# Kernel tuning notes

Measured on AMD Instinct MI355X. Metric: run time of the kernel, lower is better.

## Reference

```python
import jax, jax.numpy as jnp
import numpy as np

EPS = 1e-8  # F.cosine_similarity default eps
THRESHOLD = 0.5
NUM_PROTOTYPES = 64
W_DIV_ZP = 1.0
W_DIV_PZ = 1.0
W_DIV_PP = 1.0
W_NUM = 1.0
W_CLUSTER = 1.0
W_SEP = 1.0  # NOTE: original forward applies this weight to cluster_loss (upstream bug), replicated here


def setup_inputs() -> dict:
    key = jax.random.key(0)
    k1, k2, k3, k4, k5 = jax.random.split(key, 5)
    N, IN_DIM, P, D = 4096, 768, NUM_PROTOTYPES, 256
    x = jax.random.normal(k1, (N, IN_DIM), dtype=jnp.float32)
    labels = jax.random.randint(k2, (N,), 0, 2, dtype=jnp.int64)
    # nn.Linear(input_dim, prototype_dim): W stored as [D, IN] in torch; use [IN, D] for x @ W
    bound = 1.0 / np.sqrt(IN_DIM)
    W = jax.random.uniform(k3, (IN_DIM, D), minval=-bound, maxval=bound, dtype=jnp.float32)
    b = jax.random.uniform(k4, (D,), minval=-bound, maxval=bound, dtype=jnp.float32)
    prototypes = jax.random.normal(k5, (P, D), dtype=jnp.float32)
    return {"x": x, "labels": labels, "W": W, "b": b, "prototypes": prototypes}


def _cdist(a, b):
    # Euclidean pairwise distances [Na, Nb]
    d2 = (jnp.sum(a * a, -1)[:, None] + jnp.sum(b * b, -1)[None, :]
          - 2.0 * (a @ b.T))
    return jnp.sqrt(jnp.maximum(d2, 0.0))


def _forward(x, labels, W, b, prototypes):
    P = prototypes.shape[0]
    P_pos = P // 2
    z = x @ W + b  # [N, D]

    zn = z / jnp.maximum(jnp.linalg.norm(z, axis=-1, keepdims=True), EPS)
    pn = prototypes / jnp.maximum(jnp.linalg.norm(prototypes, axis=-1, keepdims=True), EPS)
    cos = zn @ pn.T  # [N, P] cosine similarities

    token_sequences = cos[:, :, None] * prototypes[None, :, :]  # [N, P, D]

    dist = _cdist(z, prototypes)  # [N, P]

    # diversity_loss_z_p: nearest sample per prototype
    ni = jnp.argmin(dist, axis=0)  # [P]
    l_zp = jnp.mean(jnp.linalg.norm(z[ni] - prototypes, axis=-1))

    # diversity_loss_p_z: nearest prototype per sample (intended semantics)
    nj = jnp.argmin(dist, axis=1)  # [N]
    l_pz = jnp.mean(jnp.linalg.norm(z - prototypes[nj], axis=-1))

    # diversity_loss_p_p: mean pairwise prototype distance excluding diagonal
    pp = _cdist(prototypes, prototypes)
    off = 1.0 - jnp.eye(P, dtype=pp.dtype)
    l_pp = jnp.sum(pp * off) / (P * (P - 1))

    # loss_num_prototypes: penalize samples similar to > P/4 prototypes
    num_sim = jnp.sum((cos > THRESHOLD).astype(jnp.float32), axis=1)
    l_num = jnp.sum((num_sim > P / 4).astype(jnp.float32))

    # cluster_loss: 1 - max similarity to own-class prototypes, mean over all samples
    max_pos = jnp.max(cos[:, :P_pos], axis=1)
    max_neg = jnp.max(cos[:, P_pos:], axis=1)
    d_cl = jnp.where(labels == 1, 1.0 - max_pos, 1.0 - max_neg)
    l_cluster = jnp.mean(d_cl)

    loss = (W_DIV_ZP * l_zp + W_DIV_PZ * l_pz + W_DIV_PP * l_pp
            + W_NUM * l_num + W_CLUSTER * l_cluster + W_SEP * l_cluster)
    return token_sequences, loss


def reference(x, labels, W, b, prototypes):
    return _forward(x, labels, W, b, prototypes)
```

## Files before the change

kernel.cpp:

```cpp
#include <hip/hip_runtime.h>

#define NS 4096
#define IND 768
#define PP 64
#define DD 256
#define EPSF 1e-8f
#define KHALF 384

typedef float f32x4 __attribute__((ext_vector_type(4)));

__global__ __launch_bounds__(256) void k_pre(const float* __restrict__ x,
                                             const float* __restrict__ W,
                                             const float* __restrict__ protos,
                                             float* __restrict__ z0,
                                             float* __restrict__ z1,
                                             float* __restrict__ pnorm,
                                             float* __restrict__ ppsum,
                                             unsigned int* __restrict__ minu,
                                             float* __restrict__ accum) {
    __shared__ float As[16][68];
    __shared__ float Bs[16][68];
    int tid = threadIdx.x;
    int bid = blockIdx.x;

    if (bid >= 512) {
        int p = bid - 512;
        int lane = tid & 63, w = tid >> 6;
        if (w == 0) {
            float s = 0.f;
            for (int d = lane; d < DD; d += 64) { float v = protos[p * DD + d]; s += v * v; }
#pragma unroll
            for (int o = 1; o < 64; o <<= 1) s += __shfl_xor(s, o);
            if (lane == 0) pnorm[p] = sqrtf(s);
        }
        int q = tid >> 2, quarter = tid & 3;
        const float* pr = protos + p * DD + quarter * 64;
        const float* qr = protos + q * DD + quarter * 64;
        float s2 = 0.f;
        for (int d = 0; d < 64; ++d) { float diff = pr[d] - qr[d]; s2 += diff * diff; }
        s2 += __shfl_xor(s2, 1);
        s2 += __shfl_xor(s2, 2);
        float contrib = (quarter == 0 && q != p) ? sqrtf(s2) : 0.f;
#pragma unroll
        for (int o = 1; o < 64; o <<= 1) contrib += __shfl_xor(contrib, o);
        float* red = &As[0][0];
        if (lane == 0) red[w] = contrib;
        __syncthreads();
        if (tid == 0) {
            ppsum[p] = red[0] + red[1] + red[2] + red[3];
            minu[p] = 0xFFFFFFFFu;
            if (p == 0) {
                accum[0] = 0.f; accum[1] = 0.f; accum[2] = 0.f;
                ((unsigned int*)accum)[3] = 0u;
            }
        }
        return;
    }

    int bx = bid & 63, by = (bid >> 6) & 3, bz = bid >> 8;
    int m0 = bx * 64, n0 = by * 64, kbase = bz * KHALF;
    float* __restrict__ zout = bz ? z1 : z0;
    float c[4][4] = {};
    int tx = tid & 15, ty = tid >> 4;
    int am = tid >> 2, ak = (tid & 3) * 4;
    int bk = tid >> 4, bn = (tid & 15) * 4;
    const float* xp = x + (size_t)(m0 + am) * IND + kbase + ak;
    const float* wp = W + (size_t)(kbase + bk) * DD + n0 + bn;

    f32x4 ra = *(const f32x4*)xp;
    f32x4 rb = *(const f32x4*)wp;

    for (int k0 = 0; k0 < KHALF; k0 += 16) {
        As[ak + 0][am] = ra.x;
        As[ak + 1][am] = ra.y;
        As[ak + 2][am] = ra.z;
        As[ak + 3][am] = ra.w;
        *(f32x4*)&Bs[bk][bn] = rb;
        __syncthreads();
        if (k0 + 16 < KHALF) {
            ra = *(const f32x4*)(xp + k0 + 16);
            rb = *(const f32x4*)(wp + (size_t)(k0 + 16) * DD);
        }
#pragma unroll
        for (int k = 0; k < 16; ++k) {
            float a[4], bb[4];
#pragma unroll
            for (int i = 0; i < 4; ++i) a[i] = As[k][ty * 4 + i];
#pragma unroll
            for (int j = 0; j < 4; ++j) bb[j] = Bs[k][tx * 4 + j];
#pragma unroll
            for (int i = 0; i < 4; ++i)
#pragma unroll
                for (int j = 0; j < 4; ++j) c[i][j] += a[i] * bb[j];
        }
        __syncthreads();
    }
#pragma unroll
    for (int i = 0; i < 4; ++i) {
        int m = m0 + ty * 4 + i;
        f32x4 rv = {c[i][0], c[i][1], c[i][2], c[i][3]};
        *(f32x4*)&zout[(size_t)m * DD + n0 + tx * 4] = rv;
    }
}

__global__ __launch_bounds__(256) void k_cosw(const float* __restrict__ z0,
                                              const float* __restrict__ z1,
                                              const float* __restrict__ bias,
                                              const float* __restrict__ protos,
                                              const float* __restrict__ pnorm,
                                              const int* __restrict__ labels,
                                              float* __restrict__ out,
                                              unsigned int* __restrict__ minu,
                                              float* __restrict__ accum,
                                              const float* __restrict__ ppsum,
                                              int out_last) {
    __shared__ f32x4 protoT4[PP * 64];
    __shared__ __align__(16) float rowbuf[4][2][DD];
    __shared__ float wmin[4][64];
    __shared__ float wacc[4][3];
    int tid = threadIdx.x;
    const f32x4* pr4g = (const f32x4*)protos;
    for (int idx = tid; idx < PP * 64; idx += 256) {
        int pp = idx >> 6, db = idx & 63;
        protoT4[pp * 64 + (db ^ (pp & 7))] = pr4g[idx];
    }

    int w = tid >> 6, lane = tid & 63;
    int p = lane;
    float pn = pnorm[p];
    float pn2 = pn * pn;
    float4 b4 = ((const float4*)bias)[lane];
    int nbase = blockIdx.x * 8 + w * 2;

    float zn[2];
#pragma unroll
    for (int s = 0; s < 2; ++s) {
        int n = nbase + s;
        float4 a = ((const float4*)z0)[n * 64 + lane];
        float4 cc = ((const float4*)z1)[n * 64 + lane];
        float4 r;
        r.x = a.x + cc.x + b4.x; r.y = a.y + cc.y + b4.y;
        r.z = a.z + cc.z + b4.z; r.w = a.w + cc.w + b4.w;
        float ss = r.x * r.x + r.y * r.y + r.z * r.z + r.w * r.w;
#pragma unroll
        for (int o = 1; o < 64; o <<= 1) ss += __shfl_xor(ss, o);
        zn[s] = sqrtf(ss);
        ((float4*)rowbuf[w][s])[lane] = r;
    }
    __syncthreads();

    float dot0 = 0.f, dot1 = 0.f;
#pragma unroll 8
    for (int d4 = 0; d4 < 64; ++d4) {
        f32x4 r0 = ((const f32x4*)rowbuf[w][0])[d4];
        f32x4 r1 = ((const f32x4*)rowbuf[w][1])[d4];
        f32x4 pv = protoT4[p * 64 + (d4 ^ (p & 7))];
        dot0 += r0.x * pv.x + r0.y * pv.y + r0.z * pv.z + r0.w * pv.w;
        dot1 += r1.x * pv.x + r1.y * pv.y + r1.z * pv.z + r1.w * pv.w;
    }
    float dots[2] = {dot0, dot1};

    float cosv[2];
    float regmin = 3.4e38f;
    float s_pz = 0.f, s_cl = 0.f, s_num = 0.f;
#pragma unroll
    for (int s = 0; s < 2; ++s) {
        int n = nbase + s;
        float dot = dots[s];
        float c = dot / (fmaxf(zn[s], EPSF) * fmaxf(pn, EPSF));
        cosv[s] = c;
        float d2 = zn[s] * zn[s] + pn2 - 2.f * dot;
        float dist = sqrtf(fmaxf(d2, 0.f));
        regmin = fminf(regmin, dist);

        unsigned long long bal = __ballot(c > 0.5f);
        int cnt = __popcll(bal);

        float mind = dist;
#pragma unroll
        for (int o = 1; o < 64; o <<= 1) mind = fminf(mind, __shfl_xor(mind, o));
        float mx = c;
#pragma unroll
        for (int o = 1; o < 32; o <<= 1) mx = fmaxf(mx, __shfl_xor(mx, o));
        float max_pos = __shfl(mx, 0);
        float max_neg = __shfl(mx, 32);
        if (lane == 0) {
            float dcl = (labels[n] == 1) ? (1.f - max_pos) : (1.f - max_neg);
            s_pz += mind;
            s_cl += dcl;
            if (cnt > 16) s_num += 1.f;
        }
    }

    {
        const f32x4* pr4 = (const f32x4*)protos;
        f32x4* o0 = (f32x4*)out + (size_t)(nbase + 0) * 4096 + lane;
        f32x4* o1 = (f32x4*)out + (size_t)(nbase + 1) * 4096 + lane;
        float cv0 = cosv[0], cv1 = cosv[1];
#pragma unroll 8
        for (int pp = 0; pp < 64; ++pp) {
            f32x4 v = pr4[pp * 64 + lane];
            float c0 = __shfl(cv0, pp);
            float c1 = __shfl(cv1, pp);
            __builtin_nontemporal_store(c0 * v, &o0[pp * 64]);
            __builtin_nontemporal_store(c1 * v, &o1[pp * 64]);
        }
    }

    wmin[w][lane] = regmin;
    if (lane == 0) { wacc[w][0] = s_pz; wacc[w][1] = s_cl; wacc[w][2] = s_num; }
    __syncthreads();
    if (w == 0) {
        float m = fminf(fminf(wmin[0][lane], wmin[1][lane]),
                        fminf(wmin[2][lane], wmin[3][lane]));
        atomicMin(&minu[lane], __float_as_uint(m));
        if (lane == 0) {
            atomicAdd(&accum[0], wacc[0][0] + wacc[1][0] + wacc[2][0] + wacc[3][0]);
            atomicAdd(&accum[1], wacc[0][1] + wacc[1][1] + wacc[2][1] + wacc[3][1]);
            atomicAdd(&accum[2], wacc[0][2] + wacc[1][2] + wacc[2][2] + wacc[3][2]);
        }
        __threadfence();
        unsigned int t = 0;
        if (lane == 0) t = atomicAdd((unsigned int*)accum + 3, 1u);
        t = __shfl(t, 0);
        if (t == 511u) {
            __threadfence();
            float mv = __uint_as_float(atomicMin(&minu[lane], 0xFFFFFFFFu));
            float v = mv * (1.f / PP) + ppsum[lane] * (1.f / (PP * (PP - 1)));
#pragma unroll
            for (int o = 1; o < 64; o <<= 1) v += __shfl_xor(v, o);
            if (lane == 0) {
                float l_pz = atomicAdd(&accum[0], 0.f) * (1.f / NS);
                float l_cl = atomicAdd(&accum[1], 0.f) * (1.f / NS);
                float l_num = atomicAdd(&accum[2], 0.f);
                out[out_last] = v + l_pz + l_num + 2.f * l_cl;
            }
        }
    }
}

extern "C" void kernel_launch(void* const* d_in, const int* in_sizes, int n_in,
                              void* d_out, int out_size, void* d_ws, size_t ws_size,
                              hipStream_t stream) {
    const float* x      = (const float*)d_in[0];
    const int*   labels = (const int*)d_in[1];
    const float* W      = (const float*)d_in[2];
    const float* bias   = (const float*)d_in[3];
    const float* protos = (const float*)d_in[4];
    float* out = (float*)d_out;
    float* ws = (float*)d_ws;

    float* z0    = ws;
    float* z1    = ws + 1048576;
    float* pnorm = ws + 2097152;
    float* ppsum = pnorm + 64;
    unsigned int* minu = (unsigned int*)(ppsum + 64);
    float* accum = (float*)(minu + 64);

    k_pre<<<576, 256, 0, stream>>>(x, W, protos, z0, z1, pnorm, ppsum, minu, accum);
    k_cosw<<<512, 256, 0, stream>>>(z0, z1, bias, protos, pnorm, labels, out,
                                    minu, accum, ppsum, out_size - 1);
}
```

Measured before the change: 343.7 us.

## Fuse projection GEMM into cosine/output kernel, drop z workspace round trip

Replaces the two-kernel pipeline (split-K tiled GEMM writing partial z to workspace, then cosine/output kernel) with one fused kernel. Each block computes its 8 rows of z directly, with each thread owning one output column and streaming the W column and x rows, then keeps z in shared memory for the cosine, distance and output stages. Prototype norms are computed inline and pairwise prototype distances are accumulated atomically by the first 64 blocks, while memsets replace the initializer blocks. This removes the z global write/read and one launch, but the GEMM loses shared-memory tiling: W is reread by every block with strided loads and there is no split-K, so GEMM efficiency may drop.

```diff
diff --git a/kernel.cpp b/kernel.cpp
--- a/kernel.cpp
+++ b/kernel.cpp
@@ -5,159 +5,86 @@
 #define PP 64
 #define DD 256
 #define EPSF 1e-8f
-#define KHALF 384
 
 typedef float f32x4 __attribute__((ext_vector_type(4)));
 
-__global__ __launch_bounds__(256) void k_pre(const float* __restrict__ x,
-                                             const float* __restrict__ W,
-                                             const float* __restrict__ protos,
-                                             float* __restrict__ z0,
-                                             float* __restrict__ z1,
-                                             float* __restrict__ pnorm,
-                                             float* __restrict__ ppsum,
-                                             unsigned int* __restrict__ minu,
-                                             float* __restrict__ accum) {
-    __shared__ float As[16][68];
-    __shared__ float Bs[16][68];
-    int tid = threadIdx.x;
-    int bid = blockIdx.x;
-
-    if (bid >= 512) {
-        int p = bid - 512;
-        int lane = tid & 63, w = tid >> 6;
-        if (w == 0) {
-            float s = 0.f;
-            for (int d = lane; d < DD; d += 64) { float v = protos[p * DD + d]; s += v * v; }
-#pragma unroll
-            for (int o = 1; o < 64; o <<= 1) s += __shfl_xor(s, o);
-            if (lane == 0) pnorm[p] = sqrtf(s);
-        }
-        int q = tid >> 2, quarter = tid & 3;
-        const float* pr = protos + p * DD + quarter * 64;
-        const float* qr = protos + q * DD + quarter * 64;
-        float s2 = 0.f;
-        for (int d = 0; d < 64; ++d) { float diff = pr[d] - qr[d]; s2 += diff * diff; }
-        s2 += __shfl_xor(s2, 1);
-        s2 += __shfl_xor(s2, 2);
-        float contrib = (quarter == 0 && q != p) ? sqrtf(s2) : 0.f;
-#pragma unroll
-        for (int o = 1; o < 64; o <<= 1) contrib += __shfl_xor(contrib, o);
-        float* red = &As[0][0];
-        if (lane == 0) red[w] = contrib;
-        __syncthreads();
-        if (tid == 0) {
-            ppsum[p] = red[0] + red[1] + red[2] + red[3];
-            minu[p] = 0xFFFFFFFFu;
-            if (p == 0) {
-                accum[0] = 0.f; accum[1] = 0.f; accum[2] = 0.f;
-                ((unsigned int*)accum)[3] = 0u;
-            }
-        }
-        return;
-    }
-
-    int bx = bid & 63, by = (bid >> 6) & 3, bz = bid >> 8;
-    int m0 = bx * 64, n0 = by * 64, kbase = bz * KHALF;
-    float* __restrict__ zout = bz ? z1 : z0;
-    float c[4][4] = {};
-    int tx = tid & 15, ty = tid >> 4;
-    int am = tid >> 2, ak = (tid & 3) * 4;
-    int bk = tid >> 4, bn = (tid & 15) * 4;
-    const float* xp = x + (size_t)(m0 + am) * IND + kbase + ak;
-    const float* wp = W + (size_t)(kbase + bk) * DD + n0 + bn;
-
-    f32x4 ra = *(const f32x4*)xp;
-    f32x4 rb = *(const f32x4*)wp;
-
-    for (int k0 = 0; k0 < KHALF; k0 += 16) {
-        As[ak + 0][am] = ra.x;
-        As[ak + 1][am] = ra.y;
-        As[ak + 2][am] = ra.z;
-        As[ak + 3][am] = ra.w;
-        *(f32x4*)&Bs[bk][bn] = rb;
-        __syncthreads();
-        if (k0 + 16 < KHALF) {
-            ra = *(const f32x4*)(xp + k0 + 16);
-            rb = *(const f32x4*)(wp + (size_t)(k0 + 16) * DD);
-        }
-#pragma unroll
-        for (int k = 0; k < 16; ++k) {
-            float a[4], bb[4];
-#pragma unroll
-            for (int i = 0; i < 4; ++i) a[i] = As[k][ty * 4 + i];
-#pragma unroll
-            for (int j = 0; j < 4; ++j) bb[j] = Bs[k][tx * 4 + j];
-#pragma unroll
-            for (int i = 0; i < 4; ++i)
-#pragma unroll
-                for (int j = 0; j < 4; ++j) c[i][j] += a[i] * bb[j];
-        }
-        __syncthreads();
-    }
-#pragma unroll
-    for (int i = 0; i < 4; ++i) {
-        int m = m0 + ty * 4 + i;
-        f32x4 rv = {c[i][0], c[i][1], c[i][2], c[i][3]};
-        *(f32x4*)&zout[(size_t)m * DD + n0 + tx * 4] = rv;
-    }
-}
-
-__global__ __launch_bounds__(256) void k_cosw(const float* __restrict__ z0,
-                                              const float* __restrict__ z1,
-                                              const float* __restrict__ bias,
-                                              const float* __restrict__ protos,
-                                              const float* __restrict__ pnorm,
-                                              const int* __restrict__ labels,
-                                              float* __restrict__ out,
-                                              unsigned int* __restrict__ minu,
-                                              float* __restrict__ accum,
-                                              const float* __restrict__ ppsum,
-                                              int out_last) {
+__global__ __launch_bounds__(256) void k_fused(const float* __restrict__ x,
+                                               const float* __restrict__ W,
+                                               const float* __restrict__ bias,
+                                               const float* __restrict__ protos,
+                                               const int* __restrict__ labels,
+                                               float* __restrict__ out,
+                                               unsigned int* __restrict__ minu,
+                                               float* __restrict__ accum,
+                                               int out_last) {
     __shared__ f32x4 protoT4[PP * 64];
-    __shared__ __align__(16) float rowbuf[4][2][DD];
+    __shared__ __align__(16) float rowbuf[8][DD];
     __shared__ float wmin[4][64];
     __shared__ float wacc[4][3];
     int tid = threadIdx.x;
+    int bid = blockIdx.x;
+    int nbase = bid * 8;
+
     const f32x4* pr4g = (const f32x4*)protos;
     for (int idx = tid; idx < PP * 64; idx += 256) {
         int pp = idx >> 6, db = idx & 63;
         protoT4[pp * 64 + (db ^ (pp & 7))] = pr4g[idx];
     }
 
+    float bv = bias[tid];
+
+    const float* xr = x + (size_t)nbase * IND;
+    const float* wp = W + tid;
+    float c[8] = {};
+    f32x4 xv[8];
+    float w0, w1, w2, w3;
+#pragma unroll
+    for (int r = 0; r < 8; ++r) xv[r] = *(const f32x4*)&xr[r * IND];
+    w0 = wp[0 * DD]; w1 = wp[1 * DD]; w2 = wp[2 * DD]; w3 = wp[3 * DD];
+    for (int k4 = 0; k4 < IND / 4; ++k4) {
+        f32x4 cx[8];
+        float cw0 = w0, cw1 = w1, cw2 = w2, cw3 = w3;
+#pragma unroll
+        for (int r = 0; r < 8; ++r) cx[r] = xv[r];
+        if (k4 + 1 < IND / 4) {
+            int k = (k4 + 1) * 4;
+#pragma unroll
+            for (int r = 0; r < 8; ++r) xv[r] = *(const f32x4*)&xr[r * IND + k];
+            w0 = wp[(size_t)(k + 0) * DD]; w1 = wp[(size_t)(k + 1) * DD];
+            w2 = wp[(size_t)(k + 2) * DD]; w3 = wp[(size_t)(k + 3) * DD];
+        }
+#pragma unroll
+        for (int r = 0; r < 8; ++r)
+            c[r] += cx[r].x * cw0 + cx[r].y * cw1 + cx[r].z * cw2 + cx[r].w * cw3;
+    }
+#pragma unroll
+    for (int r = 0; r < 8; ++r) rowbuf[r][tid] = c[r] + bv;
+    __syncthreads();
+
     int w = tid >> 6, lane = tid & 63;
     int p = lane;
-    float pn = pnorm[p];
-    float pn2 = pn * pn;
-    float4 b4 = ((const float4*)bias)[lane];
-    int nbase = blockIdx.x * 8 + w * 2;
 
     float zn[2];
 #pragma unroll
     for (int s = 0; s < 2; ++s) {
-        int n = nbase + s;
-        float4 a = ((const float4*)z0)[n * 64 + lane];
-        float4 cc = ((const float4*)z1)[n * 64 + lane];
-        float4 r;
-        r.x = a.x + cc.x + b4.x; r.y = a.y + cc.y + b4.y;
-        r.z = a.z + cc.z + b4.z; r.w = a.w + cc.w + b4.w;
-        float ss = r.x * r.x + r.y * r.y + r.z * r.z + r.w * r.w;
+        f32x4 r4 = ((const f32x4*)rowbuf[2 * w + s])[lane];
+        float ss = r4.x * r4.x + r4.y * r4.y + r4.z * r4.z + r4.w * r4.w;
 #pragma unroll
         for (int o = 1; o < 64; o <<= 1) ss += __shfl_xor(ss, o);
         zn[s] = sqrtf(ss);
-        ((float4*)rowbuf[w][s])[lane] = r;
-    }
-    __syncthreads();
-
-    float dot0 = 0.f, dot1 = 0.f;
+    }
+
+    float dot0 = 0.f, dot1 = 0.f, pp2 = 0.f;
 #pragma unroll 8
     for (int d4 = 0; d4 < 64; ++d4) {
-        f32x4 r0 = ((const f32x4*)rowbuf[w][0])[d4];
-        f32x4 r1 = ((const f32x4*)rowbuf[w][1])[d4];
+        f32x4 r0 = ((const f32x4*)rowbuf[2 * w + 0])[d4];
+        f32x4 r1 = ((const f32x4*)rowbuf[2 * w + 1])[d4];
         f32x4 pv = protoT4[p * 64 + (d4 ^ (p & 7))];
         dot0 += r0.x * pv.x + r0.y * pv.y + r0.z * pv.z + r0.w * pv.w;
         dot1 += r1.x * pv.x + r1.y * pv.y + r1.z * pv.z + r1.w * pv.w;
-    }
+        pp2  += pv.x * pv.x + pv.y * pv.y + pv.z * pv.z + pv.w * pv.w;
+    }
+    float pn = sqrtf(pp2);
     float dots[2] = {dot0, dot1};
 
     float cosv[2];
@@ -165,21 +92,21 @@
     float s_pz = 0.f, s_cl = 0.f, s_num = 0.f;
 #pragma unroll
     for (int s = 0; s < 2; ++s) {
-        int n = nbase + s;
+        int n = nbase + 2 * w + s;
         float dot = dots[s];
-        float c = dot / (fmaxf(zn[s], EPSF) * fmaxf(pn, EPSF));
-        cosv[s] = c;
-        float d2 = zn[s] * zn[s] + pn2 - 2.f * dot;
+        float cs = dot / (fmaxf(zn[s], EPSF) * fmaxf(pn, EPSF));
+        cosv[s] = cs;
+        float d2 = zn[s] * zn[s] + pp2 - 2.f * dot;
         float dist = sqrtf(fmaxf(d2, 0.f));
         regmin = fminf(regmin, dist);
 
-        unsigned long long bal = __ballot(c > 0.5f);
+        unsigned long long bal = __ballot(cs > 0.5f);
         int cnt = __popcll(bal);
 
         float mind = dist;
 #pragma unroll
         for (int o = 1; o < 64; o <<= 1) mind = fminf(mind, __shfl_xor(mind, o));
-        float mx = c;
+        float mx = cs;
 #pragma unroll
         for (int o = 1; o < 32; o <<= 1) mx = fmaxf(mx, __shfl_xor(mx, o));
         float max_pos = __shfl(mx, 0);
@@ -194,8 +121,8 @@
 
     {
         const f32x4* pr4 = (const f32x4*)protos;
-        f32x4* o0 = (f32x4*)out + (size_t)(nbase + 0) * 4096 + lane;
-        f32x4* o1 = (f32x4*)out + (size_t)(nbase + 1) * 4096 + lane;
+        f32x4* o0 = (f32x4*)out + (size_t)(nbase + 2 * w + 0) * 4096 + lane;
+        f32x4* o1 = (f32x4*)out + (size_t)(nbase + 2 * w + 1) * 4096 + lane;
         float cv0 = cosv[0], cv1 = cosv[1];
 #pragma unroll 8
         for (int pp = 0; pp < 64; ++pp) {
@@ -219,21 +146,40 @@
             atomicAdd(&accum[1], wacc[0][1] + wacc[1][1] + wacc[2][1] + wacc[3][1]);
             atomicAdd(&accum[2], wacc[0][2] + wacc[1][2] + wacc[2][2] + wacc[3][2]);
         }
+    }
+
+    if (bid < PP) {
+        int q = tid >> 2, quarter = tid & 3;
+        const float* pr = protos + bid * DD + quarter * 64;
+        const float* qr = protos + q * DD + quarter * 64;
+        float s2 = 0.f;
+        for (int d = 0; d < 64; ++d) { float diff = pr[d] - qr[d]; s2 += diff * diff; }
+        s2 += __shfl_xor(s2, 1);
+        s2 += __shfl_xor(s2, 2);
+        float contrib = (quarter == 0 && q != bid) ? sqrtf(s2) : 0.f;
+#pragma unroll
+        for (int o = 1; o < 64; o <<= 1) contrib += __shfl_xor(contrib, o);
+        if (lane == 0) atomicAdd(&accum[3], contrib);
+    }
+
+    __syncthreads();
+    if (w == 0) {
         __threadfence();
         unsigned int t = 0;
-        if (lane == 0) t = atomicAdd((unsigned int*)accum + 3, 1u);
+        if (lane == 0) t = atomicAdd((unsigned int*)accum + 4, 1u);
         t = __shfl(t, 0);
         if (t == 511u) {
             __threadfence();
             float mv = __uint_as_float(atomicMin(&minu[lane], 0xFFFFFFFFu));
-            float v = mv * (1.f / PP) + ppsum[lane] * (1.f / (PP * (PP - 1)));
+            float v = mv * (1.f / PP);
 #pragma unroll
             for (int o = 1; o < 64; o <<= 1) v += __shfl_xor(v, o);
             if (lane == 0) {
+                float l_pp = atomicAdd(&accum[3], 0.f) * (1.f / (PP * (PP - 1)));
                 float l_pz = atomicAdd(&accum[0], 0.f) * (1.f / NS);
                 float l_cl = atomicAdd(&accum[1], 0.f) * (1.f / NS);
                 float l_num = atomicAdd(&accum[2], 0.f);
-                out[out_last] = v + l_pz + l_num + 2.f * l_cl;
+                out[out_last] = v + l_pp + l_pz + l_num + 2.f * l_cl;
             }
         }
     }
@@ -250,14 +196,11 @@
     float* out = (float*)d_out;
     float* ws = (float*)d_ws;
 
-    float* z0    = ws;
-    float* z1    = ws + 1048576;
-    float* pnorm = ws + 2097152;
-    float* ppsum = pnorm + 64;
-    unsigned int* minu = (unsigned int*)(ppsum + 64);
-    float* accum = (float*)(minu + 64);
-
-    k_pre<<<576, 256, 0, stream>>>(x, W, protos, z0, z1, pnorm, ppsum, minu, accum);
-    k_cosw<<<512, 256, 0, stream>>>(z0, z1, bias, protos, pnorm, labels, out,
-                                    minu, accum, ppsum, out_size - 1);
+    unsigned int* minu = (unsigned int*)ws;
+    float* accum = ws + 64;
+
+    hipMemsetAsync(minu, 0xFF, 64 * sizeof(unsigned int), stream);
+    hipMemsetAsync(accum, 0, 5 * sizeof(float), stream);
+    k_fused<<<512, 256, 0, stream>>>(x, W, bias, protos, labels, out,
+                                     minu, accum, out_size - 1);
 }
```

Result: slower. 384.1 us (+11.8%).
